# Kernel tuning notes

Measured on AMD Instinct MI355X. Metric: run time of the kernel, lower is better.

The kernel has to match this reference:

```python
import jax, jax.numpy as jnp
import numpy as np

B, T, DM, DQ, DA, F, K = 128, 1024, 512, 1024, 128, 32, 31


def setup_inputs() -> dict:
    key = jax.random.key(0)
    ks = jax.random.split(key, 9)
    state = jax.random.uniform(ks[1], (B, T), dtype=jnp.float32)
    state = state / jnp.sum(state, axis=-1, keepdims=True)  # alignment-like
    return {
        "query": jax.random.normal(ks[0], (B, DQ), dtype=jnp.float32),
        "state": state,
        "prev_max_alignments": jax.random.randint(ks[2], (B,), 0, T, dtype=jnp.int32),
        "memory": jax.random.normal(ks[3], (B, T, DM), dtype=jnp.float32),
        "Wq": jax.random.normal(ks[4], (DQ, DA), dtype=jnp.float32) * 0.02,
        "Wmem": jax.random.normal(ks[5], (DM, DA), dtype=jnp.float32) * 0.02,
        "conv_k": jax.random.normal(ks[6], (K, 1, F), dtype=jnp.float32) * 0.02,
        "Wloc": jax.random.normal(ks[7], (F, DA), dtype=jnp.float32) * 0.02,
        "v_w": jax.random.normal(ks[8], (DA,), dtype=jnp.float32) * 0.02,
        "v_b": jnp.zeros((), dtype=jnp.float32),
    }


def reference(query, state, prev_max_alignments, memory, Wq, Wmem, conv_k, Wloc, v_w, v_b):
    # processed query: [B, 1, DA]
    pq = (query @ Wq)[:, None, :]
    # location features: Conv1D 'same', no bias, over cumulative alignments [B, T, 1]
    f = jax.lax.conv_general_dilated(
        state[:, :, None], conv_k,
        window_strides=(1,), padding="SAME",
        dimension_numbers=("NWC", "WIO", "NWC"),
    )  # [B, T, F]
    loc = f @ Wloc                      # [B, T, DA]
    keys = memory @ Wmem                # [B, T, DA]
    # additive tanh score -> [B, T]
    energy = jnp.tanh(keys + pq + loc) @ v_w + v_b
    alignments = jax.nn.softmax(energy, axis=-1)
    new_state = alignments + state      # is_cumulate=True
    # context: [B, DM]
    context = jnp.einsum("bt,btd->bd", alignments, memory)
    return context, alignments, new_state
```

## Files before the change

### kernel.cpp

```cpp
#include <hip/hip_runtime.h>
#include <math.h>

#define B  128
#define T  1024
#define DM 512
#define DQ 1024
#define DA 128
#define F  32
#define KW 31
#define TSEG 4

typedef short s16x8 __attribute__((ext_vector_type(8)));
typedef float f32x4 __attribute__((ext_vector_type(4)));
typedef unsigned int u32;
typedef __attribute__((address_space(1))) const unsigned int gu32;
typedef __attribute__((address_space(3))) unsigned int lu32;

__device__ __forceinline__ unsigned short f2bf(float f) {
    u32 u = __builtin_bit_cast(u32, f);
    u32 r = u + 0x7FFFu + ((u >> 16) & 1u);
    return (unsigned short)(r >> 16);
}
__device__ __forceinline__ float bf2f(unsigned short h) {
    u32 u = ((u32)h) << 16;
    return __builtin_bit_cast(float, u);
}
__device__ __forceinline__ float fast_tanh(float x) {
    float ax = fabsf(x);
    float e = __expf(-2.0f * ax);
    float t = 1.0f - 2.0f * e / (1.0f + e);
    return copysignf(t, x);
}

__global__ __launch_bounds__(128) void prep_kernel(
        const float* __restrict__ query, const float* __restrict__ Wq,
        const float* __restrict__ Wmem, const float* __restrict__ conv_k,
        const float* __restrict__ Wloc,
        float* __restrict__ pq, unsigned short* __restrict__ wsplit,
        unsigned short* __restrict__ CWt) {
    int a = threadIdx.x;
    int blk = blockIdx.x;
    if (blk < B) {
        const float* q = query + blk * DQ;
        float s = 0.f;
        for (int i = 0; i < DQ; ++i) s += q[i] * Wq[i * DA + a];
        pq[blk * DA + a] = s;
    } else if (blk < B + DM) {
        int k = blk - B;
        float w0 = Wmem[k * DA + a];
        unsigned short hi = f2bf(w0);
        float d = w0 - bf2f(hi);
        unsigned short lo = f2bf(d);
        int c = k >> 6;
        int es = (k & 63) ^ ((a & 7) << 3);
        int base = c * 16384 + a * 64 + es;
        wsplit[base] = hi;
        wsplit[base + 8192] = lo;
    } else {
        int k = blk - (B + DM);
        float s = 0.f;
        if (k < KW) {
            #pragma unroll
            for (int f = 0; f < F; ++f) s += conv_k[k * F + f] * Wloc[f * DA + a];
        }
        CWt[a * 32 + k] = f2bf(s);
    }
}

__global__ __launch_bounds__(256, 3) void energy_mfma(
        const float* __restrict__ memory, const float* __restrict__ state,
        const float* __restrict__ pq, const unsigned short* __restrict__ wsplit,
        const unsigned short* __restrict__ CWt, const float* __restrict__ v_w,
        const float* __restrict__ v_b, float* __restrict__ energy) {
    __shared__ unsigned short Wlds[16384];
    __shared__ float stl[160];
    __shared__ float pql[DA];
    __shared__ float vwl[DA];

    int tid = threadIdx.x;
    int w = tid >> 6, l = tid & 63, r = l & 15, g = l >> 4;
    int b  = blockIdx.x >> 3;
    int t0 = (blockIdx.x & 7) << 7;

    for (int i = tid; i < 160; i += 256) {
        int t = t0 - 15 + i;
        stl[i] = (i < 159 && t >= 0 && t < T) ? state[b * T + t] : 0.f;
    }
    if (tid < DA) { pql[tid] = pq[b * DA + tid]; vwl[tid] = v_w[tid]; }

    f32x4 acc0[8], acc1[8];
    #pragma unroll
    for (int nt = 0; nt < 8; ++nt) {
        acc0[nt] = (f32x4){0.f, 0.f, 0.f, 0.f};
        acc1[nt] = (f32x4){0.f, 0.f, 0.f, 0.f};
    }

    const int swz8 = (r & 7) << 3;
    const size_t arow = ((size_t)(b * T + t0 + w * 32 + r)) * DM;

    for (int c = 0; c < 8; ++c) {
        __syncthreads();
        {
            const unsigned short* src = wsplit + (size_t)c * 16384 + tid * 8;
            #pragma unroll
            for (int rd = 0; rd < 8; ++rd)
                __builtin_amdgcn_global_load_lds((gu32*)(src + rd * 2048),
                                                 (lu32*)(Wlds + (w << 9) + rd * 2048),
                                                 16, 0, 0);
        }
        __syncthreads();

        const float* Ab = memory + arow + c * 64;
        #pragma unroll
        for (int kk = 0; kk < 2; ++kk) {
            const float* p0 = Ab + kk * 32 + g * 8;
            f32x4 f00 = *(const f32x4*)p0;
            f32x4 f01 = *(const f32x4*)(p0 + 4);
            const float* p1 = p0 + 16 * DM;
            f32x4 f10 = *(const f32x4*)p1;
            f32x4 f11 = *(const f32x4*)(p1 + 4);
            s16x8 Ah0, Al0, Ah1, Al1;
            #pragma unroll
            for (int j = 0; j < 4; ++j) {
                unsigned short h;
                h = f2bf(f00[j]); Ah0[j]     = (short)h; Al0[j]     = (short)f2bf(f00[j] - bf2f(h));
                h = f2bf(f01[j]); Ah0[4 + j] = (short)h; Al0[4 + j] = (short)f2bf(f01[j] - bf2f(h));
                h = f2bf(f10[j]); Ah1[j]     = (short)h; Al1[j]     = (short)f2bf(f10[j] - bf2f(h));
                h = f2bf(f11[j]); Ah1[4 + j] = (short)h; Al1[4 + j] = (short)f2bf(f11[j] - bf2f(h));
            }
            int off = (kk * 32 + g * 8) ^ swz8;
            #pragma unroll
            for (int nt = 0; nt < 8; ++nt) {
                const unsigned short* bp = Wlds + (nt * 16 + r) * 64 + off;
                s16x8 Bh = *(const s16x8*)bp;
                s16x8 Bl = *(const s16x8*)(bp + 8192);
                acc0[nt] = __builtin_amdgcn_mfma_f32_16x16x32_bf16(Ah0, Bh, acc0[nt], 0, 0, 0);
                acc0[nt] = __builtin_amdgcn_mfma_f32_16x16x32_bf16(Ah0, Bl, acc0[nt], 0, 0, 0);
                acc0[nt] = __builtin_amdgcn_mfma_f32_16x16x32_bf16(Al0, Bh, acc0[nt], 0, 0, 0);
                acc1[nt] = __builtin_amdgcn_mfma_f32_16x16x32_bf16(Ah1, Bh, acc1[nt], 0, 0, 0);
                acc1[nt] = __builtin_amdgcn_mfma_f32_16x16x32_bf16(Ah1, Bl, acc1[nt], 0, 0, 0);
                acc1[nt] = __builtin_amdgcn_mfma_f32_16x16x32_bf16(Al1, Bh, acc1[nt], 0, 0, 0);
            }
        }
    }

    __syncthreads();
    #pragma unroll
    for (int rd = 0; rd < 2; ++rd)
        __builtin_amdgcn_global_load_lds((gu32*)(CWt + rd * 2048 + tid * 8),
                                         (lu32*)(Wlds + (w << 9) + rd * 2048),
                                         16, 0, 0);
    __syncthreads();

    s16x8 st0, st1;
    {
        int base0 = w * 32 + r + g * 8;
        #pragma unroll
        for (int j = 0; j < 8; ++j) {
            st0[j] = (short)f2bf(stl[base0 + j]);
            st1[j] = (short)f2bf(stl[base0 + 16 + j]);
        }
    }
    #pragma unroll
    for (int nt = 0; nt < 8; ++nt) {
        const unsigned short* cp = Wlds + (nt * 16 + r) * 32 + g * 8;
        s16x8 cw = *(const s16x8*)cp;
        acc0[nt] = __builtin_amdgcn_mfma_f32_16x16x32_bf16(st0, cw, acc0[nt], 0, 0, 0);
        acc1[nt] = __builtin_amdgcn_mfma_f32_16x16x32_bf16(st1, cw, acc1[nt], 0, 0, 0);
    }

    float vb = *v_b;
    #pragma unroll
    for (int sub = 0; sub < 2; ++sub) {
        #pragma unroll
        for (int reg = 0; reg < 4; ++reg) {
            float p = 0.f;
            #pragma unroll
            for (int nt = 0; nt < 8; ++nt) {
                int col = nt * 16 + r;
                float v = (sub == 0) ? acc0[nt][reg] : acc1[nt][reg];
                p += fast_tanh(v + pql[col]) * vwl[col];
            }
            p += __shfl_xor(p, 1, 16);
            p += __shfl_xor(p, 2, 16);
            p += __shfl_xor(p, 4, 16);
            p += __shfl_xor(p, 8, 16);
            if (r == 0)
                energy[b * T + t0 + w * 32 + sub * 16 + g * 4 + reg] = p + vb;
        }
    }
}

__global__ __launch_bounds__(256) void softmax_kernel(
        const float* __restrict__ energy, const float* __restrict__ state,
        float* __restrict__ alignments, float* __restrict__ new_state) {
    int b = blockIdx.x;
    int tid = threadIdx.x;
    __shared__ float rmax[4], rsum[4];
    float4 ev = ((const float4*)(energy + b * T))[tid];
    float m = fmaxf(fmaxf(ev.x, ev.y), fmaxf(ev.z, ev.w));
    #pragma unroll
    for (int off = 32; off > 0; off >>= 1) m = fmaxf(m, __shfl_xor(m, off, 64));
    if ((tid & 63) == 0) rmax[tid >> 6] = m;
    __syncthreads();
    m = fmaxf(fmaxf(rmax[0], rmax[1]), fmaxf(rmax[2], rmax[3]));
    float4 x;
    x.x = __expf(ev.x - m); x.y = __expf(ev.y - m);
    x.z = __expf(ev.z - m); x.w = __expf(ev.w - m);
    float s = x.x + x.y + x.z + x.w;
    #pragma unroll
    for (int off = 32; off > 0; off >>= 1) s += __shfl_xor(s, off, 64);
    if ((tid & 63) == 0) rsum[tid >> 6] = s;
    __syncthreads();
    s = rsum[0] + rsum[1] + rsum[2] + rsum[3];
    float inv = 1.0f / s;
    float4 st4 = ((const float4*)(state + b * T))[tid];
    float4 al = make_float4(x.x * inv, x.y * inv, x.z * inv, x.w * inv);
    ((float4*)(alignments + b * T))[tid] = al;
    float4 ns = make_float4(al.x + st4.x, al.y + st4.y, al.z + st4.z, al.w + st4.w);
    ((float4*)(new_state + b * T))[tid] = ns;
}

__global__ __launch_bounds__(256) void context_partial_kernel(
        const float* __restrict__ memory, const float* __restrict__ alignments,
        float* __restrict__ partial) {
    int b = blockIdx.x;
    int seg = blockIdx.y;
    int tid = threadIdx.x;
    __shared__ float al[T / TSEG];
    int t0 = seg * (T / TSEG);
    al[tid] = alignments[b * T + t0 + tid];
    __syncthreads();
    const float* memB = memory + (size_t)b * T * DM + (size_t)t0 * DM;
    float acc0 = 0.f, acc1 = 0.f;
    #pragma unroll 4
    for (int t = 0; t < T / TSEG; ++t) {
        float a = al[t];
        acc0 += a * memB[(size_t)t * DM + tid];
        acc1 += a * memB[(size_t)t * DM + tid + 256];
    }
    partial[((size_t)seg * B + b) * DM + tid] = acc0;
    partial[((size_t)seg * B + b) * DM + tid + 256] = acc1;
}

__global__ __launch_bounds__(256) void context_reduce_kernel(
        const float* __restrict__ partial, float* __restrict__ context) {
    int b = blockIdx.x;
    int tid = threadIdx.x;
    #pragma unroll
    for (int j = 0; j < 2; ++j) {
        int d = tid + j * 256;
        float s = 0.f;
        #pragma unroll
        for (int g = 0; g < TSEG; ++g) s += partial[((size_t)g * B + b) * DM + d];
        context[b * DM + d] = s;
    }
}

extern "C" void kernel_launch(void* const* d_in, const int* in_sizes, int n_in,
                              void* d_out, int out_size, void* d_ws, size_t ws_size,
                              hipStream_t stream) {
    const float* query  = (const float*)d_in[0];
    const float* state  = (const float*)d_in[1];
    const float* memory = (const float*)d_in[3];
    const float* Wq     = (const float*)d_in[4];
    const float* Wmem   = (const float*)d_in[5];
    const float* conv_k = (const float*)d_in[6];
    const float* Wloc   = (const float*)d_in[7];
    const float* v_w    = (const float*)d_in[8];
    const float* v_b    = (const float*)d_in[9];

    float* out        = (float*)d_out;
    float* context    = out;
    float* alignments = out + B * DM;
    float* new_state  = out + B * DM + B * T;

    char* ws = (char*)d_ws;
    float*          pq      = (float*)ws;
    unsigned short* wsplit  = (unsigned short*)(ws + 65536);
    unsigned short* CWt     = (unsigned short*)(ws + 327680);
    float*          energy  = (float*)(ws + 335872);
    float*          partial = (float*)(ws + 860160);

    prep_kernel<<<dim3(B + DM + 32), 128, 0, stream>>>(query, Wq, Wmem, conv_k, Wloc, pq, wsplit, CWt);
    energy_mfma<<<dim3(B * (T / 128)), 256, 0, stream>>>(memory, state, pq, wsplit, CWt, v_w, v_b, energy);
    softmax_kernel<<<dim3(B), 256, 0, stream>>>(energy, state, alignments, new_state);
    context_partial_kernel<<<dim3(B, TSEG), 256, 0, stream>>>(memory, alignments, partial);
    context_reduce_kernel<<<dim3(B), 256, 0, stream>>>(partial, context);
}
```

Before: 144.1 us.

## Split query projection four ways and fuse softmax into context partial kernel

The query projection in the prep kernel is split into four K-chunks across more blocks, and the energy kernel sums the four partials when it loads pq. This shortens the serial 1024-long dot product per thread. Softmax is fused into the context-partial kernel: each of the four segment blocks recomputes the full-row softmax, writes its own quarter of alignments and new_state, then reads memory with float4 loads split across two half-block groups. This removes one kernel launch and the alignments round trip, at the cost of redundant softmax work per segment and a small extra reduction through shared memory.

```diff
diff --git a/kernel.cpp b/kernel.cpp
--- a/kernel.cpp
+++ b/kernel.cpp
@@ -36,17 +36,20 @@
         const float* __restrict__ query, const float* __restrict__ Wq,
         const float* __restrict__ Wmem, const float* __restrict__ conv_k,
         const float* __restrict__ Wloc,
-        float* __restrict__ pq, unsigned short* __restrict__ wsplit,
+        float* __restrict__ pqp, unsigned short* __restrict__ wsplit,
         unsigned short* __restrict__ CWt) {
     int a = threadIdx.x;
     int blk = blockIdx.x;
-    if (blk < B) {
-        const float* q = query + blk * DQ;
+    if (blk < 4 * B) {
+        int b = blk >> 2, q = blk & 3;
+        const float* qp = query + b * DQ + q * 256;
+        const float* wp = Wq + (size_t)(q * 256) * DA + a;
         float s = 0.f;
-        for (int i = 0; i < DQ; ++i) s += q[i] * Wq[i * DA + a];
-        pq[blk * DA + a] = s;
-    } else if (blk < B + DM) {
-        int k = blk - B;
+        #pragma unroll 4
+        for (int i = 0; i < 256; ++i) s += qp[i] * wp[(size_t)i * DA];
+        pqp[(q * B + b) * DA + a] = s;
+    } else if (blk < 4 * B + DM) {
+        int k = blk - 4 * B;
         float w0 = Wmem[k * DA + a];
         unsigned short hi = f2bf(w0);
         float d = w0 - bf2f(hi);
@@ -57,7 +60,7 @@
         wsplit[base] = hi;
         wsplit[base + 8192] = lo;
     } else {
-        int k = blk - (B + DM);
+        int k = blk - (4 * B + DM);
         float s = 0.f;
         if (k < KW) {
             #pragma unroll
@@ -69,7 +72,7 @@
 
 __global__ __launch_bounds__(256, 3) void energy_mfma(
         const float* __restrict__ memory, const float* __restrict__ state,
-        const float* __restrict__ pq, const unsigned short* __restrict__ wsplit,
+        const float* __restrict__ pqp, const unsigned short* __restrict__ wsplit,
         const unsigned short* __restrict__ CWt, const float* __restrict__ v_w,
         const float* __restrict__ v_b, float* __restrict__ energy) {
     __shared__ unsigned short Wlds[16384];
@@ -86,7 +89,13 @@
         int t = t0 - 15 + i;
         stl[i] = (i < 159 && t >= 0 && t < T) ? state[b * T + t] : 0.f;
     }
-    if (tid < DA) { pql[tid] = pq[b * DA + tid]; vwl[tid] = v_w[tid]; }
+    if (tid < DA) {
+        float s = 0.f;
+        #pragma unroll
+        for (int q = 0; q < 4; ++q) s += pqp[(q * B + b) * DA + tid];
+        pql[tid] = s;
+        vwl[tid] = v_w[tid];
+    }
 
     f32x4 acc0[8], acc1[8];
     #pragma unroll
@@ -191,56 +200,59 @@
     }
 }
 
-__global__ __launch_bounds__(256) void softmax_kernel(
+__global__ __launch_bounds__(256) void softmax_context_kernel(
         const float* __restrict__ energy, const float* __restrict__ state,
-        float* __restrict__ alignments, float* __restrict__ new_state) {
-    int b = blockIdx.x;
-    int tid = threadIdx.x;
+        const float* __restrict__ memory,
+        float* __restrict__ alignments, float* __restrict__ new_state,
+        float* __restrict__ partial) {
+    int b = blockIdx.x, seg = blockIdx.y, tid = threadIdx.x;
     __shared__ float rmax[4], rsum[4];
-    float4 ev = ((const float4*)(energy + b * T))[tid];
-    float m = fmaxf(fmaxf(ev.x, ev.y), fmaxf(ev.z, ev.w));
+    __shared__ float al[T / TSEG];
+    __shared__ f32x4 comb[128];
+
+    f32x4 ev = ((const f32x4*)(energy + b * T))[tid];
+    float m = fmaxf(fmaxf(ev[0], ev[1]), fmaxf(ev[2], ev[3]));
     #pragma unroll
     for (int off = 32; off > 0; off >>= 1) m = fmaxf(m, __shfl_xor(m, off, 64));
     if ((tid & 63) == 0) rmax[tid >> 6] = m;
     __syncthreads();
     m = fmaxf(fmaxf(rmax[0], rmax[1]), fmaxf(rmax[2], rmax[3]));
-    float4 x;
-    x.x = __expf(ev.x - m); x.y = __expf(ev.y - m);
-    x.z = __expf(ev.z - m); x.w = __expf(ev.w - m);
-    float s = x.x + x.y + x.z + x.w;
+    f32x4 x;
+    x[0] = __expf(ev[0] - m); x[1] = __expf(ev[1] - m);
+    x[2] = __expf(ev[2] - m); x[3] = __expf(ev[3] - m);
+    float s = x[0] + x[1] + x[2] + x[3];
     #pragma unroll
     for (int off = 32; off > 0; off >>= 1) s += __shfl_xor(s, off, 64);
     if ((tid & 63) == 0) rsum[tid >> 6] = s;
     __syncthreads();
     s = rsum[0] + rsum[1] + rsum[2] + rsum[3];
     float inv = 1.0f / s;
-    float4 st4 = ((const float4*)(state + b * T))[tid];
-    float4 al = make_float4(x.x * inv, x.y * inv, x.z * inv, x.w * inv);
-    ((float4*)(alignments + b * T))[tid] = al;
-    float4 ns = make_float4(al.x + st4.x, al.y + st4.y, al.z + st4.z, al.w + st4.w);
-    ((float4*)(new_state + b * T))[tid] = ns;
-}
-
-__global__ __launch_bounds__(256) void context_partial_kernel(
-        const float* __restrict__ memory, const float* __restrict__ alignments,
-        float* __restrict__ partial) {
-    int b = blockIdx.x;
-    int seg = blockIdx.y;
-    int tid = threadIdx.x;
-    __shared__ float al[T / TSEG];
-    int t0 = seg * (T / TSEG);
-    al[tid] = alignments[b * T + t0 + tid];
-    __syncthreads();
-    const float* memB = memory + (size_t)b * T * DM + (size_t)t0 * DM;
-    float acc0 = 0.f, acc1 = 0.f;
+    f32x4 a4 = x * inv;
+    if ((tid >> 6) == seg) {
+        ((f32x4*)al)[tid & 63] = a4;
+        ((f32x4*)(alignments + b * T))[tid] = a4;
+        f32x4 st4 = ((const f32x4*)(state + b * T))[tid];
+        ((f32x4*)(new_state + b * T))[tid] = a4 + st4;
+    }
+    __syncthreads();
+
+    int half = tid >> 7;
+    int dg = tid & 127;
+    const float* memB = memory + ((size_t)b * T + seg * (T / TSEG)) * DM;
+    f32x4 acc = (f32x4){0.f, 0.f, 0.f, 0.f};
     #pragma unroll 4
-    for (int t = 0; t < T / TSEG; ++t) {
+    for (int it = 0; it < 128; ++it) {
+        int t = it * 2 + half;
         float a = al[t];
-        acc0 += a * memB[(size_t)t * DM + tid];
-        acc1 += a * memB[(size_t)t * DM + tid + 256];
-    }
-    partial[((size_t)seg * B + b) * DM + tid] = acc0;
-    partial[((size_t)seg * B + b) * DM + tid + 256] = acc1;
+        f32x4 v = *(const f32x4*)(memB + (size_t)t * DM + dg * 4);
+        acc += v * a;
+    }
+    if (half) comb[dg] = acc;
+    __syncthreads();
+    if (!half) {
+        acc += comb[dg];
+        ((f32x4*)(partial + ((size_t)seg * B + b) * DM))[dg] = acc;
+    }
 }
 
 __global__ __launch_bounds__(256) void context_reduce_kernel(
@@ -276,15 +288,14 @@
     float* new_state  = out + B * DM + B * T;
 
     char* ws = (char*)d_ws;
-    float*          pq      = (float*)ws;
-    unsigned short* wsplit  = (unsigned short*)(ws + 65536);
-    unsigned short* CWt     = (unsigned short*)(ws + 327680);
-    float*          energy  = (float*)(ws + 335872);
-    float*          partial = (float*)(ws + 860160);
-
-    prep_kernel<<<dim3(B + DM + 32), 128, 0, stream>>>(query, Wq, Wmem, conv_k, Wloc, pq, wsplit, CWt);
-    energy_mfma<<<dim3(B * (T / 128)), 256, 0, stream>>>(memory, state, pq, wsplit, CWt, v_w, v_b, energy);
-    softmax_kernel<<<dim3(B), 256, 0, stream>>>(energy, state, alignments, new_state);
-    context_partial_kernel<<<dim3(B, TSEG), 256, 0, stream>>>(memory, alignments, partial);
+    float*          pqp     = (float*)ws;
+    unsigned short* wsplit  = (unsigned short*)(ws + 262144);
+    unsigned short* CWt     = (unsigned short*)(ws + 524288);
+    float*          energy  = (float*)(ws + 532480);
+    float*          partial = (float*)(ws + 1056768);
+
+    prep_kernel<<<dim3(4 * B + DM + 32), 128, 0, stream>>>(query, Wq, Wmem, conv_k, Wloc, pqp, wsplit, CWt);
+    energy_mfma<<<dim3(B * (T / 128)), 256, 0, stream>>>(memory, state, pqp, wsplit, CWt, v_w, v_b, energy);
+    softmax_context_kernel<<<dim3(B, TSEG), 256, 0, stream>>>(energy, state, memory, alignments, new_state, partial);
     context_reduce_kernel<<<dim3(B), 256, 0, stream>>>(partial, context);
 }
```

Result: faster. 135.0 us (-6.3%).
